# Performance work log

Measured on AMD Instinct MI355X. Metric: run time of the kernel, lower is better.

The kernel has to match this reference:

```python
import jax, jax.numpy as jnp
import numpy as np

DN = ('NCHW', 'OIHW', 'NCHW')
SCALES = (4, 2, 5, 2, 1914)  # per-feature one-hot widths; sum=1927, +1 scalar row = 1928 CNN channels


def conv(x, w, b, stride):
    y = jax.lax.conv_general_dilated(x, w, stride, 'VALID', dimension_numbers=DN)
    return y + b[None, :, None, None]


def maxpool(x, window):
    return jax.lax.reduce_window(x, -jnp.inf, jax.lax.max, (1, 1) + window, (1, 1) + window, 'VALID')


def setup_inputs() -> dict:
    key = jax.random.key(0)
    ks = jax.random.split(key, 16)
    B, T, F, H, W = 2, 32, 8, 128, 128
    replay = jax.random.randint(ks[0], (B, T, F, H, W), 0, 2).astype(jnp.float32)

    def rn(k, shape, scale=0.02):
        return jax.random.normal(k, shape, jnp.float32) * scale

    return dict(
        replay_tensor=replay,
        emb_table=rn(ks[1], (16384, 200), 1.0),
        conv_con_w=rn(ks[2], (1, 1, 4, 4)), conv_con_b=jnp.zeros((1,), jnp.float32),
        fc_con_w=rn(ks[3], (200, 961)), fc_con_b=jnp.zeros((200,), jnp.float32),
        cnn1_w=rn(ks[4], (964, 1928, 1, 2)), cnn1_b=jnp.zeros((964,), jnp.float32),
        cnn2_w=rn(ks[5], (482, 964, 1, 2)), cnn2_b=jnp.zeros((482,), jnp.float32),
        cnn3_w=rn(ks[6], (241, 482, 1, 2)), cnn3_b=jnp.zeros((241,), jnp.float32),
        cnn4_w=rn(ks[7], (100, 241, 1, 2)), cnn4_b=jnp.zeros((100,), jnp.float32),
        fc_cnn_w=rn(ks[8], (100, 2300)), fc_cnn_b=jnp.zeros((100,), jnp.float32),
        lstm_w_ih=rn(ks[9], (400, 100), 0.1), lstm_w_hh=rn(ks[10], (400, 100), 0.1),
        lstm_b_ih=jnp.zeros((400,), jnp.float32), lstm_b_hh=jnp.zeros((400,), jnp.float32),
        fc_out_w=rn(ks[11], (2, 100), 0.1), fc_out_b=jnp.zeros((2,), jnp.float32),
        batch_size=2,
    )


def reference(replay_tensor, emb_table, conv_con_w, conv_con_b, fc_con_w, fc_con_b,
              cnn1_w, cnn1_b, cnn2_w, cnn2_b, cnn3_w, cnn3_b, cnn4_w, cnn4_b,
              fc_cnn_w, fc_cnn_b, lstm_w_ih, lstm_w_hh, lstm_b_ih, lstm_b_hh,
              fc_out_w, fc_out_b, batch_size):
    # np.delete(replay, 2, 2) then np.delete(., 3, 2) removes original features 2 and 4
    replay = replay_tensor[:batch_size, :, jnp.array([0, 1, 3, 5, 6, 7])]
    B, T = replay.shape[0], replay.shape[1]
    scalar = replay[:, :, 0]   # [B,T,128,128]
    cat = replay[:, :, 1:6]    # [B,T,5,128,128]

    # --- categorical branch ---
    # The original builds a [scale_k, H*W] one-hot scatter per (b,t,k), then the
    # embedding step reads only spatial column 0: row s of the per-feature block is
    # emb_table[1] iff value_at_pos0 == s (nonzero after thresholding), else emb_table[0].
    v0 = cat[:, :, :, 0, 0].astype(jnp.int32)  # [B,T,5]
    embs = []
    for k, sc in enumerate(SCALES):
        v = v0[:, :, k]
        v = jnp.where(v > sc, 0, v)  # threshold: values > scale_ zeroed
        idx = ((jnp.arange(sc)[None, None, :] == v[:, :, None]) & (v[:, :, None] != 0)).astype(jnp.int32)
        embs.append(emb_table[idx])  # [B,T,sc,200]
    emb_full = jnp.concatenate(embs, axis=2)  # [B,T,1927,200]

    # --- scalar conv branch (faithful to the bug: cnn_con2 applied to raw x) ---
    x = scalar.reshape(B * T, 1, 128, 128)
    y = maxpool(jax.nn.relu(conv(x, conv_con_w, conv_con_b, (2, 2))), (2, 2))  # [BT,1,31,31]
    y = y.reshape(B * T, -1) @ fc_con_w.T + fc_con_b                           # [BT,200]
    sca_full = y.reshape(B, T, 1, 200)

    # --- CNN over concatenated [1928, 1, 200] frames ---
    z = jnp.concatenate([sca_full, emb_full], axis=2).reshape(B * T, 1928, 1, 200)
    z = maxpool(jax.nn.relu(conv(z, cnn1_w, cnn1_b, (1, 1))), (1, 2))
    z = maxpool(jax.nn.relu(conv(z, cnn2_w, cnn2_b, (1, 1))), (1, 2))
    z = maxpool(jax.nn.relu(conv(z, cnn3_w, cnn3_b, (1, 1))), (1, 2))
    z = jax.nn.relu(conv(z, cnn4_w, cnn4_b, (1, 1)))  # [BT,100,1,23]
    z = z.reshape(B * T, -1) @ fc_cnn_w.T + fc_cnn_b  # [BT,100]
    seq = z.reshape(B, T, 100)

    # --- single-layer LSTM (torch gate order i,f,g,o), zero init state ---
    def step(carry, x_t):
        h, c = carry
        g = x_t @ lstm_w_ih.T + h @ lstm_w_hh.T + lstm_b_ih + lstm_b_hh
        i, f, gg, o = jnp.split(g, 4, axis=-1)
        c = jax.nn.sigmoid(f) * c + jax.nn.sigmoid(i) * jnp.tanh(gg)
        h = jax.nn.sigmoid(o) * jnp.tanh(c)
        return (h, c), None

    h0 = jnp.zeros((B, 100), seq.dtype)
    c0 = jnp.zeros((B, 100), seq.dtype)
    (hT, _), _ = jax.lax.scan(step, (h0, c0), jnp.swapaxes(seq, 0, 1))
    return hT @ fc_out_w.T + fc_out_b  # [B,2]
```

## Files before the change

kernel.cpp:

```cpp
#include <hip/hip_runtime.h>
#include <math.h>

#define DEVFN __device__ __forceinline__

typedef __bf16 bf16x8 __attribute__((ext_vector_type(8)));
typedef float f32x4 __attribute__((ext_vector_type(4)));

constexpr int T_ = 32;
constexpr int HW = 128;
constexpr int C1IN = 1928;
constexpr int C1 = 964;

DEVFN float sigm(float x) { return 1.0f / (1.0f + __expf(-x)); }

DEVFN ushort f2b(float v) {
    union { float f; unsigned u; } x; x.f = v;
    unsigned r = x.u + 0x7fffu + ((x.u >> 16) & 1u);
    return (ushort)(r >> 16);
}

DEVFN void gload16(const ushort* g, ushort* l) {
    __builtin_amdgcn_global_load_lds(
        (const __attribute__((address_space(1))) unsigned int*)g,
        (__attribute__((address_space(3))) unsigned int*)l, 16, 0, 0);
}

__global__ void k_sca_conv(const float* __restrict__ replay, const float* __restrict__ wc,
                           const float* __restrict__ bc, float* __restrict__ y) {
    const int n = blockIdx.x;
    const int idx = blockIdx.y * 256 + threadIdx.x;
    if (idx >= 961) return;
    const float* x = replay + (size_t)n * 8 * HW * HW;
    float wr_[16];
    #pragma unroll
    for (int t = 0; t < 16; ++t) wr_[t] = wc[t];
    const float bcv = bc[0];
    const int i = idx / 31, j = idx % 31;
    float m = 0.0f;
    #pragma unroll
    for (int di = 0; di < 2; ++di)
    #pragma unroll
    for (int dj = 0; dj < 2; ++dj) {
        const int h0 = 2 * (2 * i + di), w0 = 2 * (2 * j + dj);
        float acc = bcv;
        #pragma unroll
        for (int p = 0; p < 4; ++p)
        #pragma unroll
        for (int q = 0; q < 4; ++q)
            acc += x[(h0 + p) * HW + (w0 + q)] * wr_[p * 4 + q];
        m = fmaxf(m, fmaxf(acc, 0.0f));
    }
    y[n * 961 + idx] = m;
}

__global__ void k_sca_fc(const float* __restrict__ y, const float* __restrict__ fcw,
                         const float* __restrict__ fcb, float* __restrict__ sca) {
    const int n = blockIdx.x;
    const int wid = threadIdx.x >> 6, lane = threadIdx.x & 63;
    const int o = blockIdx.y * 4 + wid;
    float acc = 0.f;
    for (int m = lane; m < 961; m += 64)
        acc += y[n * 961 + m] * fcw[(size_t)o * 961 + m];
    #pragma unroll
    for (int off = 32; off > 0; off >>= 1) acc += __shfl_down(acc, off);
    if (lane == 0) sca[n * 200 + o] = acc + fcb[o];
}

__global__ void k_wsum(const float* __restrict__ w1, float* __restrict__ wsum) {
    const int oc = blockIdx.x;
    const float* wr = w1 + (size_t)oc * C1IN * 2;
    float s0 = 0.f, s1 = 0.f;
    for (int ic = threadIdx.x; ic < C1IN; ic += 64) {
        s0 += wr[ic * 2 + 0];
        s1 += wr[ic * 2 + 1];
    }
    #pragma unroll
    for (int off = 32; off > 0; off >>= 1) {
        s0 += __shfl_down(s0, off);
        s1 += __shfl_down(s1, off);
    }
    if (threadIdx.x == 0) { wsum[oc * 2] = s0; wsum[oc * 2 + 1] = s1; }
}

__global__ void k_sa(const float* __restrict__ replay, const float* __restrict__ w1,
                     float* __restrict__ sa) {
    const int n = blockIdx.y;
    const int oc = blockIdx.x * blockDim.x + threadIdx.x;
    if (oc >= C1) return;
    const int chs[5]    = {1, 3, 5, 6, 7};
    const int scales[5] = {4, 2, 5, 2, 1914};
    const int offs[5]   = {0, 4, 6, 11, 13};
    float s0 = 0.f, s1 = 0.f;
    #pragma unroll
    for (int k = 0; k < 5; ++k) {
        int v = (int)replay[((size_t)n * 8 + chs[k]) * HW * HW];
        if (v > scales[k]) v = 0;
        if (v >= 1 && v <= scales[k] - 1) {
            const int ic = 1 + offs[k] + v;
            s0 += w1[((size_t)oc * C1IN + ic) * 2 + 0];
            s1 += w1[((size_t)oc * C1IN + ic) * 2 + 1];
        }
    }
    sa[(n * C1 + oc) * 2 + 0] = s0;
    sa[(n * C1 + oc) * 2 + 1] = s1;
}

template <int OCT>
__global__ void k_cnn1(const float* __restrict__ sca, const float* __restrict__ emb,
                       const float* __restrict__ w1, const float* __restrict__ b1,
                       const float* __restrict__ wsum, const float* __restrict__ sa,
                       ushort* __restrict__ Bt2) {
    const int n = blockIdx.x;
    const int ocBase = blockIdx.y * OCT;
    const int tx = threadIdx.x;
    __shared__ float ev[200], sv[200], dv[200];
    __shared__ float oscal[OCT][7];
    __shared__ float vals[OCT][100];
    for (int i = tx; i < 200; i += blockDim.x) {
        const float e0 = emb[i], e1 = emb[200 + i];
        ev[i] = e0;
        dv[i] = e1 - e0;
        sv[i] = sca[n * 200 + i] - e0;
    }
    for (int i = tx; i < OCT * 7; i += blockDim.x) {
        const int ocl = i / 7, f = i % 7;
        const int oc = ocBase + ocl;
        float v = 0.f;
        if (oc < C1) {
            switch (f) {
                case 0: v = wsum[oc * 2 + 0]; break;
                case 1: v = wsum[oc * 2 + 1]; break;
                case 2: v = b1[oc]; break;
                case 3: v = w1[(size_t)oc * C1IN * 2 + 0]; break;
                case 4: v = w1[(size_t)oc * C1IN * 2 + 1]; break;
                case 5: v = sa[(n * C1 + oc) * 2 + 0]; break;
                case 6: v = sa[(n * C1 + oc) * 2 + 1]; break;
            }
        }
        oscal[ocl][f] = v;
    }
    __syncthreads();
    for (int item = tx; item < OCT * 99; item += blockDim.x) {
        const int ocl = item / 99, u = item % 99;
        const int oc = ocBase + ocl;
        float res = 0.f;
        if (oc < C1) {
            const float ws0 = oscal[ocl][0], ws1 = oscal[ocl][1], bb = oscal[ocl][2];
            const float a0 = oscal[ocl][3], a1 = oscal[ocl][4];
            const float s0 = oscal[ocl][5], s1 = oscal[ocl][6];
            float r = -INFINITY;
            #pragma unroll
            for (int dw = 0; dw < 2; ++dw) {
                const int ww = 2 * u + dw;
                const float o = bb + ws0 * ev[ww] + ws1 * ev[ww + 1]
                                   + a0 * sv[ww] + a1 * sv[ww + 1]
                                   + s0 * dv[ww] + s1 * dv[ww + 1];
                r = fmaxf(r, o);
            }
            res = fmaxf(r, 0.0f);
        }
        vals[ocl][u] = res;
    }
    __syncthreads();
    for (int i = tx; i < OCT * 100; i += blockDim.x) {
        const int u = i >> 4, ocl = i & 15;
        const float v = (u < 99) ? vals[ocl][u] : 0.0f;
        Bt2[(size_t)(n * 100 + u) * 1024 + ocBase + ocl] = f2b(v);
    }
    if (n == 0 && ocBase == 0) {
        for (int i = tx; i < 1024; i += blockDim.x)
            Bt2[(size_t)6400 * 1024 + i] = 0;
    }
}

__global__ void k_prep_w(const float* __restrict__ w2, const float* __restrict__ w3,
                         const float* __restrict__ w4, const float* __restrict__ whh,
                         ushort* __restrict__ A2, ushort* __restrict__ A3,
                         ushort* __restrict__ A4, float* __restrict__ whhT) {
    const int idx = blockIdx.x * 256 + threadIdx.x;
    constexpr int N2 = 2 * 512 * 1024;
    constexpr int N3 = 2 * 256 * 512;
    constexpr int N4 = 2 * 128 * 256;
    if (idx < N2) {
        const int kw = idx >> 19;
        const int r = idx & 524287;
        const int oc = r >> 10, ic = r & 1023;
        const float v = (oc < 482 && ic < 964) ? w2[(size_t)oc * 1928 + ic * 2 + kw] : 0.f;
        A2[idx] = f2b(v);
    } else if (idx < N2 + N3) {
        const int j = idx - N2;
        const int kw = j >> 17;
        const int r = j & 131071;
        const int oc = r >> 9, ic = r & 511;
        const float v = (oc < 241 && ic < 482) ? w3[(size_t)oc * 964 + ic * 2 + kw] : 0.f;
        A3[j] = f2b(v);
    } else if (idx < N2 + N3 + N4) {
        const int j = idx - (N2 + N3);
        const int kw = j >> 15;
        const int r = j & 32767;
        const int oc = r >> 8, ic = r & 255;
        const float v = (oc < 100 && ic < 241) ? w4[(size_t)oc * 482 + ic * 2 + kw] : 0.f;
        A4[j] = f2b(v);
    } else {
        const int j = idx - (N2 + N3 + N4);
        if (j < 40000) {
            const int m = j / 400, p = j - m * 400;
            const int go = (p & 3) * 100 + (p >> 2);
            whhT[m * 400 + p] = whh[go * 100 + m];
        }
    }
}

template <int OCREAL, int WR, int WOUT, int KICP, int MPAD, int OMODE, int OSTR,
          bool POOL, int MT, int NTILES>
__global__ __launch_bounds__(256, 2) void k_gemm_conv(
    const ushort* __restrict__ A, const ushort* __restrict__ Bt,
    const float* __restrict__ bias, void* __restrict__ outv) {
    constexpr int BK = 64;
    constexpr int NT = KICP / BK;
    constexpr int NWG = MT * NTILES;
    constexpr int Qq = NWG / 8, Rr = NWG % 8;

    __shared__ __align__(16) ushort As0[2][4096];
    __shared__ __align__(16) ushort As1[2][4096];
    __shared__ __align__(16) ushort Bs[2][8704];

    const int bid = blockIdx.x;
    const int xcd = bid & 7, rest = bid >> 3;
    const int base = (xcd < Rr) ? xcd * (Qq + 1) : Rr * (Qq + 1) + (xcd - Rr) * Qq;
    const int sid = base + rest;
    const int mBase = (sid % MT) * 64;
    const int nBase = (sid / MT) * 128;

    const int tx = threadIdx.x;
    const int wave = tx >> 6, lane = tx & 63;
    const int lr = lane & 15, lk = lane >> 4;
    const int r8 = lane >> 3;
    const int cx = (lane & 7) ^ r8;
    const ushort* A1p = A + (size_t)MPAD * KICP;

    f32x4 acc[4][2] = {};

    auto STAGE = [&](int buf, int kt) {
        const int k0 = kt * BK + cx * 8;
        #pragma unroll
        for (int it = 0; it < 2; ++it) {
            const int s = wave + it * 4;
            const int row = s * 8 + r8;
            gload16(&A[(size_t)(mBase + row) * KICP + k0], &As0[buf][s * 512]);
            gload16(&A1p[(size_t)(mBase + row) * KICP + k0], &As1[buf][s * 512]);
        }
        #pragma unroll
        for (int it = 0; it < 4; ++it) {
            const int s = wave + it * 4;
            const int row = s * 8 + r8;
            gload16(&Bt[(size_t)(nBase + row) * KICP + k0], &Bs[buf][s * 512]);
        }
        if (wave == 0) {
            const int row = 128 + r8;
            gload16(&Bt[(size_t)(nBase + row) * KICP + k0], &Bs[buf][16 * 512]);
        }
    };

    auto COMPUTE = [&](int cur) {
        #pragma unroll
        for (int ks = 0; ks < 2; ++ks) {
            bf16x8 a0[4], a1[4], b0[2], b1[2];
            #pragma unroll
            for (int i = 0; i < 4; ++i) {
                const int row = i * 16 + lr;
                const int col = (ks * 32 + lk * 8) ^ ((row & 7) << 3);
                a0[i] = *(const bf16x8*)&As0[cur][row * 64 + col];
                a1[i] = *(const bf16x8*)&As1[cur][row * 64 + col];
            }
            #pragma unroll
            for (int j = 0; j < 2; ++j) {
                const int row = wave * 32 + j * 16 + lr;
                const int col = (ks * 32 + lk * 8) ^ ((row & 7) << 3);
                b0[j] = *(const bf16x8*)&Bs[cur][row * 64 + col];
                const int row1 = row + 1;
                const int col1 = (ks * 32 + lk * 8) ^ ((row1 & 7) << 3);
                b1[j] = *(const bf16x8*)&Bs[cur][row1 * 64 + col1];
            }
            #pragma unroll
            for (int i = 0; i < 4; ++i)
                #pragma unroll
                for (int j = 0; j < 2; ++j) {
                    acc[i][j] = __builtin_amdgcn_mfma_f32_16x16x32_bf16(a0[i], b0[j], acc[i][j], 0, 0, 0);
                    acc[i][j] = __builtin_amdgcn_mfma_f32_16x16x32_bf16(a1[i], b1[j], acc[i][j], 0, 0, 0);
                }
        }
    };

    STAGE(0, 0);
    __syncthreads();
    #pragma unroll 1
    for (int kt = 0; kt < NT; ++kt) {
        const int cur = kt & 1;
        if (kt + 1 < NT) STAGE(cur ^ 1, kt + 1);
        COMPUTE(cur);
        __syncthreads();
    }

    ushort* outb = (ushort*)outv;
    float*  outf = (float*)outv;
    constexpr int NOUTW = POOL ? (WOUT / 2) : WOUT;
    constexpr int WRN = NOUTW + 1;
    constexpr int NVALID = WR * 64;
    #pragma unroll
    for (int i = 0; i < 4; ++i) {
        const int m0 = mBase + i * 16 + lk * 4;
        #pragma unroll
        for (int j = 0; j < 2; ++j) {
            const int r = nBase + wave * 32 + j * 16 + lr;
            const int n = r / WR, w = r - n * WR;
            #pragma unroll
            for (int reg = 0; reg < 4; ++reg) {
                const float v = acc[i][j][reg];
                const float vo = __shfl_xor(v, 1);
                const int m = m0 + reg;
                const bool lok = POOL ? ((lr & 1) == 0) : true;
                if (lok && (w < WOUT) && (m < OCREAL) && (r < NVALID)) {
                    const float pre = POOL ? fmaxf(v, vo) : v;
                    const float val = fmaxf(pre + bias[m], 0.0f);
                    const int wc = POOL ? (w >> 1) : w;
                    if (OMODE == 2)
                        outb[((size_t)(n * WRN + wc)) * OSTR + m] = f2b(val);
                    else
                        outf[((size_t)n * OCREAL + m) * NOUTW + wc] = val;
                }
            }
        }
    }
}

__global__ void k_fc_cnn(const float* __restrict__ z4, const float* __restrict__ w,
                         const float* __restrict__ b, float* __restrict__ seq) {
    const int n = blockIdx.x;
    const int wid = threadIdx.x >> 6, lane = threadIdx.x & 63;
    const int o = blockIdx.y * 4 + wid;
    const float4* zr = (const float4*)(z4 + (size_t)n * 2300);
    const float4* wr = (const float4*)(w + (size_t)o * 2300);
    float acc = 0.f;
    for (int m = lane; m < 575; m += 64) {
        const float4 wv = wr[m];
        const float4 zv = zr[m];
        acc += wv.x * zv.x + wv.y * zv.y + wv.z * zv.z + wv.w * zv.w;
    }
    #pragma unroll
    for (int off = 32; off > 0; off >>= 1) acc += __shfl_down(acc, off);
    if (lane == 0) seq[n * 100 + o] = acc + b[o];
}

__global__ void k_xg(const float* __restrict__ seq, const float* __restrict__ wih,
                     const float* __restrict__ bih, const float* __restrict__ bhh,
                     float* __restrict__ xg) {
    const int n = blockIdx.x;
    __shared__ __align__(16) float s[100];
    if (threadIdx.x < 100) s[threadIdx.x] = seq[n * 100 + threadIdx.x];
    __syncthreads();
    const int p = threadIdx.x;
    if (p < 400) {
        const int go = (p & 3) * 100 + (p >> 2);
        const float4* wr = (const float4*)(wih + (size_t)go * 100);
        const float4* s4 = (const float4*)s;
        float4 a = {0.f, 0.f, 0.f, 0.f};
        #pragma unroll
        for (int m = 0; m < 25; ++m) {
            const float4 wv = wr[m];
            const float4 sv = s4[m];
            a.x += wv.x * sv.x; a.y += wv.y * sv.y;
            a.z += wv.z * sv.z; a.w += wv.w * sv.w;
        }
        xg[n * 400 + p] = bih[go] + bhh[go] + a.x + a.y + a.z + a.w;
    }
}

__global__ __launch_bounds__(512) void k_lstm(const float* __restrict__ xg,
                                              const float* __restrict__ whhT,
                                              const float* __restrict__ fw,
                                              const float* __restrict__ fb,
                                              float* __restrict__ outp) {
    const int bb = blockIdx.x;
    const int tx = threadIdx.x;
    __shared__ __align__(16) float hb[2][104];
    float wreg[100];
    if (tx < 400) {
        #pragma unroll
        for (int m = 0; m < 100; ++m) wreg[m] = whhT[m * 400 + tx];
    }
    float creg = 0.f;
    if (tx < 104) { hb[0][tx] = 0.f; hb[1][tx] = 0.f; }
    float xnext = (tx < 400) ? xg[(size_t)(bb * T_) * 400 + tx] : 0.f;
    __syncthreads();
    const int lane = tx & 63, base = lane & ~3;
    for (int t = 0; t < T_; ++t) {
        float acc = 0.f;
        if (tx < 400) {
            acc = xnext;
            if (t + 1 < T_) xnext = xg[(size_t)(bb * T_ + t + 1) * 400 + tx];
            const float4* h4 = (const float4*)&hb[t & 1][0];
            #pragma unroll
            for (int m4 = 0; m4 < 25; ++m4) {
                const float4 hv = h4[m4];
                acc += hv.x * wreg[4 * m4 + 0] + hv.y * wreg[4 * m4 + 1]
                     + hv.z * wreg[4 * m4 + 2] + hv.w * wreg[4 * m4 + 3];
            }
        }
        const float gI = __shfl(acc, base + 0);
        const float gF = __shfl(acc, base + 1);
        const float gG = __shfl(acc, base + 2);
        const float gO = __shfl(acc, base + 3);
        if (tx < 400) {
            const float cn = sigm(gF) * creg + sigm(gI) * tanhf(gG);
            creg = cn;
            if ((tx & 3) == 0) hb[(t + 1) & 1][tx >> 2] = sigm(gO) * tanhf(cn);
        }
        __syncthreads();
    }
    if (tx < 2) {
        float acc = fb[tx];
        for (int j = 0; j < 100; ++j) acc += hb[0][j] * fw[tx * 100 + j];
        outp[bb * 2 + tx] = acc;
    }
}

extern "C" void kernel_launch(void* const* d_in, const int* in_sizes, int n_in,
                              void* d_out, int out_size, void* d_ws, size_t ws_size,
                              hipStream_t stream) {
    (void)in_sizes; (void)n_in; (void)out_size; (void)ws_size;
    const float* replay = (const float*)d_in[0];
    const float* emb    = (const float*)d_in[1];
    const float* ccw    = (const float*)d_in[2];
    const float* ccb    = (const float*)d_in[3];
    const float* fcw    = (const float*)d_in[4];
    const float* fcb    = (const float*)d_in[5];
    const float* w1     = (const float*)d_in[6];
    const float* b1     = (const float*)d_in[7];
    const float* w2     = (const float*)d_in[8];
    const float* b2     = (const float*)d_in[9];
    const float* w3     = (const float*)d_in[10];
    const float* b3     = (const float*)d_in[11];
    const float* w4     = (const float*)d_in[12];
    const float* b4     = (const float*)d_in[13];
    const float* fcnw   = (const float*)d_in[14];
    const float* fcnb   = (const float*)d_in[15];
    const float* wih    = (const float*)d_in[16];
    const float* whh    = (const float*)d_in[17];
    const float* bih    = (const float*)d_in[18];
    const float* bhh    = (const float*)d_in[19];
    const float* fow    = (const float*)d_in[20];
    const float* fob    = (const float*)d_in[21];

    float* ws = (float*)d_ws;
    float*  sca  = ws + 0;
    float*  wsum = ws + 12800;
    float*  sa   = ws + 14848;
    float*  seq  = ws + 138240;
    float*  xg   = ws + 144640;
    float*  whhT = ws + 170240;
    float*  yb   = ws + 210240;
    float*  z4   = ws + 272384;
    ushort* A2   = (ushort*)(ws + 419584);
    ushort* A3   = (ushort*)(ws + 943872);
    ushort* A4   = (ushort*)(ws + 1074944);
    ushort* Bt2  = (ushort*)(ws + 1107712);
    ushort* Bt3  = (ushort*)(ws + 4385024);
    ushort* Bt4  = (ushort*)(ws + 5208320);
    float*  outp = (float*)d_out;

    k_sca_conv<<<dim3(64, 4), 256, 0, stream>>>(replay, ccw, ccb, yb);
    k_sca_fc<<<dim3(64, 50), 256, 0, stream>>>(yb, fcw, fcb, sca);
    k_wsum<<<964, 64, 0, stream>>>(w1, wsum);
    k_sa<<<dim3(4, 64), 256, 0, stream>>>(replay, w1, sa);
    k_prep_w<<<5533, 256, 0, stream>>>(w2, w3, w4, whh, A2, A3, A4, whhT);
    k_cnn1<16><<<dim3(64, 64), 256, 0, stream>>>(sca, emb, w1, b1, wsum, sa, Bt2);
    k_gemm_conv<482, 100, 98, 1024, 512, 2, 512, true, 8, 50>
        <<<400, 256, 0, stream>>>(A2, Bt2, b2, Bt3);
    k_gemm_conv<241, 50, 48, 512, 256, 2, 256, true, 4, 25>
        <<<100, 256, 0, stream>>>(A3, Bt3, b3, Bt4);
    k_gemm_conv<100, 25, 23, 256, 128, 0, 0, false, 2, 13>
        <<<26, 256, 0, stream>>>(A4, Bt4, b4, z4);
    k_fc_cnn<<<dim3(64, 25), 256, 0, stream>>>(z4, fcnw, fcnb, seq);
    k_xg<<<64, 512, 0, stream>>>(seq, wih, bih, bhh, xg);
    k_lstm<<<2, 512, 0, stream>>>(xg, whhT, fow, fob, outp);
}
```

Measured before the change: 155.3 us.

## Merge weight-prep kernels into one launch and speed up LSTM recurrence

The wsum, sa and weight-conversion kernels are combined into a single kernel that picks its role from the block index, removing two launches and their serialization gaps. The LSTM step now splits the dot product across four independent accumulators to shorten the dependency chain. Each lane applies its own gate activation before the shuffle, so one exp is computed per lane instead of several. A fast exp-based tanh replaces tanhf, and the block shrinks to 448 threads. The fast tanh loses some accuracy for large inputs.

Result: faster. 142.2 us (-8.4%).

```diff
diff --git a/kernel.cpp b/kernel.cpp
--- a/kernel.cpp
+++ b/kernel.cpp
@@ -12,6 +12,7 @@
 constexpr int C1 = 964;
 
 DEVFN float sigm(float x) { return 1.0f / (1.0f + __expf(-x)); }
+DEVFN float tanhfast(float x) { return 2.0f / (1.0f + __expf(-2.0f * x)) - 1.0f; }
 
 DEVFN ushort f2b(float v) {
     union { float f; unsigned u; } x; x.f = v;
@@ -66,43 +67,85 @@
     if (lane == 0) sca[n * 200 + o] = acc + fcb[o];
 }
 
-__global__ void k_wsum(const float* __restrict__ w1, float* __restrict__ wsum) {
-    const int oc = blockIdx.x;
-    const float* wr = w1 + (size_t)oc * C1IN * 2;
-    float s0 = 0.f, s1 = 0.f;
-    for (int ic = threadIdx.x; ic < C1IN; ic += 64) {
-        s0 += wr[ic * 2 + 0];
-        s1 += wr[ic * 2 + 1];
-    }
-    #pragma unroll
-    for (int off = 32; off > 0; off >>= 1) {
-        s0 += __shfl_down(s0, off);
-        s1 += __shfl_down(s1, off);
-    }
-    if (threadIdx.x == 0) { wsum[oc * 2] = s0; wsum[oc * 2 + 1] = s1; }
-}
-
-__global__ void k_sa(const float* __restrict__ replay, const float* __restrict__ w1,
-                     float* __restrict__ sa) {
-    const int n = blockIdx.y;
-    const int oc = blockIdx.x * blockDim.x + threadIdx.x;
-    if (oc >= C1) return;
-    const int chs[5]    = {1, 3, 5, 6, 7};
-    const int scales[5] = {4, 2, 5, 2, 1914};
-    const int offs[5]   = {0, 4, 6, 11, 13};
-    float s0 = 0.f, s1 = 0.f;
-    #pragma unroll
-    for (int k = 0; k < 5; ++k) {
-        int v = (int)replay[((size_t)n * 8 + chs[k]) * HW * HW];
-        if (v > scales[k]) v = 0;
-        if (v >= 1 && v <= scales[k] - 1) {
-            const int ic = 1 + offs[k] + v;
-            s0 += w1[((size_t)oc * C1IN + ic) * 2 + 0];
-            s1 += w1[((size_t)oc * C1IN + ic) * 2 + 1];
-        }
-    }
-    sa[(n * C1 + oc) * 2 + 0] = s0;
-    sa[(n * C1 + oc) * 2 + 1] = s1;
+__global__ void k_prep(const float* __restrict__ w1, const float* __restrict__ w2,
+                       const float* __restrict__ w3, const float* __restrict__ w4,
+                       const float* __restrict__ whh, const float* __restrict__ replay,
+                       float* __restrict__ wsum, float* __restrict__ sa,
+                       ushort* __restrict__ A2, ushort* __restrict__ A3,
+                       ushort* __restrict__ A4, float* __restrict__ whhT) {
+    const int bid = blockIdx.x;
+    const int tx = threadIdx.x;
+    constexpr int N2 = 2 * 512 * 1024;
+    constexpr int N3 = 2 * 256 * 512;
+    constexpr int N4 = 2 * 128 * 256;
+    if (bid < 5533) {
+        const int idx = bid * 256 + tx;
+        if (idx < N2) {
+            const int kw = idx >> 19;
+            const int r = idx & 524287;
+            const int oc = r >> 10, ic = r & 1023;
+            const float v = (oc < 482 && ic < 964) ? w2[(size_t)oc * 1928 + ic * 2 + kw] : 0.f;
+            A2[idx] = f2b(v);
+        } else if (idx < N2 + N3) {
+            const int j = idx - N2;
+            const int kw = j >> 17;
+            const int r = j & 131071;
+            const int oc = r >> 9, ic = r & 511;
+            const float v = (oc < 241 && ic < 482) ? w3[(size_t)oc * 964 + ic * 2 + kw] : 0.f;
+            A3[j] = f2b(v);
+        } else if (idx < N2 + N3 + N4) {
+            const int j = idx - (N2 + N3);
+            const int kw = j >> 15;
+            const int r = j & 32767;
+            const int oc = r >> 8, ic = r & 255;
+            const float v = (oc < 100 && ic < 241) ? w4[(size_t)oc * 482 + ic * 2 + kw] : 0.f;
+            A4[j] = f2b(v);
+        } else {
+            const int j = idx - (N2 + N3 + N4);
+            if (j < 40000) {
+                const int m = j / 400, p = j - m * 400;
+                const int go = (p & 3) * 100 + (p >> 2);
+                whhT[m * 400 + p] = whh[go * 100 + m];
+            }
+        }
+    } else if (bid < 5774) {
+        const int oc = (bid - 5533) * 4 + (tx >> 6);
+        const int lane = tx & 63;
+        const float* wr = w1 + (size_t)oc * C1IN * 2;
+        float s0 = 0.f, s1 = 0.f;
+        for (int ic = lane; ic < C1IN; ic += 64) {
+            s0 += wr[ic * 2 + 0];
+            s1 += wr[ic * 2 + 1];
+        }
+        #pragma unroll
+        for (int off = 32; off > 0; off >>= 1) {
+            s0 += __shfl_down(s0, off);
+            s1 += __shfl_down(s1, off);
+        }
+        if (lane == 0) { wsum[oc * 2] = s0; wsum[oc * 2 + 1] = s1; }
+    } else {
+        const int j = bid - 5774;
+        const int n = j >> 2;
+        const int oc = (j & 3) * 256 + tx;
+        if (oc < C1) {
+            const int chs[5]    = {1, 3, 5, 6, 7};
+            const int scales[5] = {4, 2, 5, 2, 1914};
+            const int offs[5]   = {0, 4, 6, 11, 13};
+            float s0 = 0.f, s1 = 0.f;
+            #pragma unroll
+            for (int k = 0; k < 5; ++k) {
+                int v = (int)replay[((size_t)n * 8 + chs[k]) * HW * HW];
+                if (v > scales[k]) v = 0;
+                if (v >= 1 && v <= scales[k] - 1) {
+                    const int ic = 1 + offs[k] + v;
+                    s0 += w1[((size_t)oc * C1IN + ic) * 2 + 0];
+                    s1 += w1[((size_t)oc * C1IN + ic) * 2 + 1];
+                }
+            }
+            sa[(n * C1 + oc) * 2 + 0] = s0;
+            sa[(n * C1 + oc) * 2 + 1] = s1;
+        }
+    }
 }
 
 template <int OCT>
@@ -173,44 +216,6 @@
     }
 }
 
-__global__ void k_prep_w(const float* __restrict__ w2, const float* __restrict__ w3,
-                         const float* __restrict__ w4, const float* __restrict__ whh,
-                         ushort* __restrict__ A2, ushort* __restrict__ A3,
-                         ushort* __restrict__ A4, float* __restrict__ whhT) {
-    const int idx = blockIdx.x * 256 + threadIdx.x;
-    constexpr int N2 = 2 * 512 * 1024;
-    constexpr int N3 = 2 * 256 * 512;
-    constexpr int N4 = 2 * 128 * 256;
-    if (idx < N2) {
-        const int kw = idx >> 19;
-        const int r = idx & 524287;
-        const int oc = r >> 10, ic = r & 1023;
-        const float v = (oc < 482 && ic < 964) ? w2[(size_t)oc * 1928 + ic * 2 + kw] : 0.f;
-        A2[idx] = f2b(v);
-    } else if (idx < N2 + N3) {
-        const int j = idx - N2;
-        const int kw = j >> 17;
-        const int r = j & 131071;
-        const int oc = r >> 9, ic = r & 511;
-        const float v = (oc < 241 && ic < 482) ? w3[(size_t)oc * 964 + ic * 2 + kw] : 0.f;
-        A3[j] = f2b(v);
-    } else if (idx < N2 + N3 + N4) {
-        const int j = idx - (N2 + N3);
-        const int kw = j >> 15;
-        const int r = j & 32767;
-        const int oc = r >> 8, ic = r & 255;
-        const float v = (oc < 100 && ic < 241) ? w4[(size_t)oc * 482 + ic * 2 + kw] : 0.f;
-        A4[j] = f2b(v);
-    } else {
-        const int j = idx - (N2 + N3 + N4);
-        if (j < 40000) {
-            const int m = j / 400, p = j - m * 400;
-            const int go = (p & 3) * 100 + (p >> 2);
-            whhT[m * 400 + p] = whh[go * 100 + m];
-        }
-    }
-}
-
 template <int OCREAL, int WR, int WOUT, int KICP, int MPAD, int OMODE, int OSTR,
           bool POOL, int MT, int NTILES>
 __global__ __launch_bounds__(256, 2) void k_gemm_conv(
@@ -376,7 +381,7 @@
     }
 }
 
-__global__ __launch_bounds__(512) void k_lstm(const float* __restrict__ xg,
+__global__ __launch_bounds__(448) void k_lstm(const float* __restrict__ xg,
                                               const float* __restrict__ whhT,
                                               const float* __restrict__ fw,
                                               const float* __restrict__ fb,
@@ -394,27 +399,32 @@
     float xnext = (tx < 400) ? xg[(size_t)(bb * T_) * 400 + tx] : 0.f;
     __syncthreads();
     const int lane = tx & 63, base = lane & ~3;
+    const int g = tx & 3;
     for (int t = 0; t < T_; ++t) {
-        float acc = 0.f;
+        float act = 0.f;
         if (tx < 400) {
-            acc = xnext;
+            float a0 = xnext, a1 = 0.f, a2 = 0.f, a3 = 0.f;
             if (t + 1 < T_) xnext = xg[(size_t)(bb * T_ + t + 1) * 400 + tx];
             const float4* h4 = (const float4*)&hb[t & 1][0];
             #pragma unroll
             for (int m4 = 0; m4 < 25; ++m4) {
                 const float4 hv = h4[m4];
-                acc += hv.x * wreg[4 * m4 + 0] + hv.y * wreg[4 * m4 + 1]
-                     + hv.z * wreg[4 * m4 + 2] + hv.w * wreg[4 * m4 + 3];
-            }
-        }
-        const float gI = __shfl(acc, base + 0);
-        const float gF = __shfl(acc, base + 1);
-        const float gG = __shfl(acc, base + 2);
-        const float gO = __shfl(acc, base + 3);
+                a0 += hv.x * wreg[4 * m4 + 0];
+                a1 += hv.y * wreg[4 * m4 + 1];
+                a2 += hv.z * wreg[4 * m4 + 2];
+                a3 += hv.w * wreg[4 * m4 + 3];
+            }
+            const float accv = (a0 + a1) + (a2 + a3);
+            act = (g == 2) ? tanhfast(accv) : sigm(accv);
+        }
+        const float aI = __shfl(act, base + 0);
+        const float aF = __shfl(act, base + 1);
+        const float aG = __shfl(act, base + 2);
+        const float aO = __shfl(act, base + 3);
         if (tx < 400) {
-            const float cn = sigm(gF) * creg + sigm(gI) * tanhf(gG);
+            const float cn = aF * creg + aI * aG;
             creg = cn;
-            if ((tx & 3) == 0) hb[(t + 1) & 1][tx >> 2] = sigm(gO) * tanhf(cn);
+            if (g == 0) hb[(t + 1) & 1][tx >> 2] = aO * tanhfast(cn);
         }
         __syncthreads();
     }
@@ -471,9 +481,8 @@
 
     k_sca_conv<<<dim3(64, 4), 256, 0, stream>>>(replay, ccw, ccb, yb);
     k_sca_fc<<<dim3(64, 50), 256, 0, stream>>>(yb, fcw, fcb, sca);
-    k_wsum<<<964, 64, 0, stream>>>(w1, wsum);
-    k_sa<<<dim3(4, 64), 256, 0, stream>>>(replay, w1, sa);
-    k_prep_w<<<5533, 256, 0, stream>>>(w2, w3, w4, whh, A2, A3, A4, whhT);
+    k_prep<<<6030, 256, 0, stream>>>(w1, w2, w3, w4, whh, replay,
+                                     wsum, sa, A2, A3, A4, whhT);
     k_cnn1<16><<<dim3(64, 64), 256, 0, stream>>>(sca, emb, w1, b1, wsum, sa, Bt2);
     k_gemm_conv<482, 100, 98, 1024, 512, 2, 512, true, 8, 50>
         <<<400, 256, 0, stream>>>(A2, Bt2, b2, Bt3);
@@ -483,5 +492,5 @@
         <<<26, 256, 0, stream>>>(A4, Bt4, b4, z4);
     k_fc_cnn<<<dim3(64, 25), 256, 0, stream>>>(z4, fcnw, fcnb, seq);
     k_xg<<<64, 512, 0, stream>>>(seq, wih, bih, bhh, xg);
-    k_lstm<<<2, 512, 0, stream>>>(xg, whhT, fow, fob, outp);
-}
+    k_lstm<<<2, 448, 0, stream>>>(xg, whhT, fow, fob, outp);
+}
```
